# Kernel optimization log

Hardware: AMD Instinct MI355X
Metric: run time of the kernel (lower is better)

The kernel has to match this reference:

```python
import jax, jax.numpy as jnp
import numpy as np

B, S, D_IN, D_HID, D_OUT, H = 2, 2048, 1024, 1024, 1024, 16
HD = D_HID // H  # head_dim = 64


def setup_inputs() -> dict:
    key = jax.random.key(0)
    ks = jax.random.split(key, 9)
    s_in = 1.0 / np.sqrt(D_IN)
    s_out = 1.0 / np.sqrt(D_OUT)
    return {
        "x": jax.random.normal(ks[0], (B, S, D_IN), dtype=jnp.float32),
        "Wq": jax.random.uniform(ks[1], (D_IN, D_HID), jnp.float32, -s_in, s_in),
        "bq": jax.random.uniform(ks[2], (D_HID,), jnp.float32, -s_in, s_in),
        "Wk": jax.random.uniform(ks[3], (D_IN, D_HID), jnp.float32, -s_in, s_in),
        "bk": jax.random.uniform(ks[4], (D_HID,), jnp.float32, -s_in, s_in),
        "Wv": jax.random.uniform(ks[5], (D_IN, D_OUT), jnp.float32, -s_in, s_in),
        "bv": jax.random.uniform(ks[6], (D_OUT,), jnp.float32, -s_in, s_in),
        "Wo": jax.random.uniform(ks[7], (D_OUT, D_OUT), jnp.float32, -s_out, s_out),
        "bo": jax.random.uniform(ks[8], (D_OUT,), jnp.float32, -s_out, s_out),
    }


def reference(x, Wq, bq, Wk, bk, Wv, bv, Wo, bo):
    b, s, _ = x.shape
    q = (x @ Wq + bq).reshape(b, s, H, HD)  # [B,S,H,HD]
    k = (x @ Wk + bk).reshape(b, s, H, HD)
    v = (x @ Wv + bv).reshape(b, s, H, HD)
    scores = jnp.einsum("bqhd,bkhd->bhqk", q, k) / jnp.sqrt(jnp.float32(HD))
    attn = jax.nn.softmax(scores, axis=-1)  # [B,H,S,S]
    ctx = jnp.einsum("bhqk,bkhd->bqhd", attn, v).reshape(b, s, D_HID)
    return ctx @ Wo + bo
```

## Files before the change

### kernel.cpp

```cpp
#include <hip/hip_runtime.h>
#include <stdint.h>

typedef __attribute__((ext_vector_type(8))) short short8v;
typedef __attribute__((ext_vector_type(4))) short short4v;
typedef __attribute__((ext_vector_type(4))) float float4v;
typedef __attribute__((ext_vector_type(4))) unsigned short ushort4v;
typedef __attribute__((ext_vector_type(4))) float floatvec4;
typedef __attribute__((ext_vector_type(2))) unsigned int uint2v;

#define DEVI __device__ __forceinline__

DEVI unsigned short f2bf(float f) {
    unsigned int u = __builtin_bit_cast(unsigned int, f);
    u += 0x7FFFu + ((u >> 16) & 1u);
    return (unsigned short)(u >> 16);
}

DEVI unsigned int pk2bf(float a, float b) {
#if defined(__has_builtin) && __has_builtin(__builtin_amdgcn_cvt_pk_bf16_f32)
    auto r = __builtin_amdgcn_cvt_pk_bf16_f32(a, b);
    unsigned int u;
    __builtin_memcpy(&u, &r, 4);
    return u;
#else
    return (unsigned int)f2bf(a) | ((unsigned int)f2bf(b) << 16);
#endif
}

DEVI float ex2(float x) {
#if defined(__has_builtin) && __has_builtin(__builtin_amdgcn_exp2f)
    return __builtin_amdgcn_exp2f(x);
#else
    return __builtin_exp2f(x);
#endif
}

typedef __attribute__((address_space(1))) void GV;
typedef __attribute__((address_space(3))) void LV;
DEVI void gl2lds16(const void* g, void* l) {
    __builtin_amdgcn_global_load_lds((GV*)g, (LV*)l, 16, 0, 0);
}

__global__ void conv_x_kernel(const float* __restrict__ x, unsigned short* __restrict__ xb) {
    const int i = (blockIdx.x * 256 + threadIdx.x) * 4;
    const floatvec4 v = *(const floatvec4*)&x[i];
    ushort4v o;
#pragma unroll
    for (int r = 0; r < 4; r++) o[r] = f2bf(v[r]);
    *(ushort4v*)&xb[i] = o;
}

__global__ void transpose_w4(const float* __restrict__ W0, const float* __restrict__ W1,
                             const float* __restrict__ W2, const float* __restrict__ W3,
                             unsigned short* __restrict__ D0, unsigned short* __restrict__ D1,
                             unsigned short* __restrict__ D2, unsigned short* __restrict__ D3) {
    __shared__ float t[32][33];
    const int tx = threadIdx.x, ty = threadIdx.y;
    const int bx = blockIdx.x, by = blockIdx.y, z = blockIdx.z;
    const float* W = (z == 0) ? W0 : (z == 1) ? W1 : (z == 2) ? W2 : W3;
    unsigned short* D = (z == 0) ? D0 : (z == 1) ? D1 : (z == 2) ? D2 : D3;
#pragma unroll
    for (int i = 0; i < 4; i++)
        t[ty + i * 8][tx] = W[(size_t)(by * 32 + ty + i * 8) * 1024 + bx * 32 + tx];
    __syncthreads();
#pragma unroll
    for (int i = 0; i < 4; i++)
        D[(size_t)(bx * 32 + ty + i * 8) * 1024 + by * 32 + tx] = f2bf(t[tx][ty + i * 8]);
}

__global__ __launch_bounds__(256, 2) void qkv_gemm(
    const unsigned short* __restrict__ X, const unsigned short* __restrict__ Wt,
    const float* __restrict__ bq, const float* __restrict__ bk, const float* __restrict__ bv,
    unsigned short* __restrict__ qb, unsigned short* __restrict__ kb,
    unsigned short* __restrict__ vtb)
{
    __shared__ __align__(16) unsigned short As[128 * 32];
    __shared__ __align__(16) unsigned short Bs[128 * 32];
    const int tid = threadIdx.x, lane = tid & 63, wv = tid >> 6;
    const int quad = lane >> 4, l16 = lane & 15;
    const int w = blockIdx.x >> 3;
    const int n0 = (blockIdx.x & 7) * 128;
    const int row0 = blockIdx.y * 128;
    const unsigned short* Wsel = Wt + (size_t)w * (1024 * 1024);

    const int srow = lane >> 2;
    const int sg = (lane & 3) ^ ((lane >> 2) & 3) ^ ((lane >> 4) & 3);
    const int scol = sg * 8;
    const int fsw = (l16 & 3) ^ ((l16 >> 2) & 3);
    const int wm = (wv >> 1) * 64, wn = (wv & 1) * 64;

    float4v acc[4][4];
#pragma unroll
    for (int i = 0; i < 4; i++)
#pragma unroll
        for (int j = 0; j < 4; j++) acc[i][j] = (float4v){0.f, 0.f, 0.f, 0.f};

    for (int k0 = 0; k0 < 1024; k0 += 32) {
        __syncthreads();
#pragma unroll
        for (int i = 0; i < 2; i++) {
            const int c = wv * 2 + i;
            gl2lds16(X + (size_t)(row0 + c * 16 + srow) * 1024 + k0 + scol, As + c * 512);
            gl2lds16(Wsel + (size_t)(n0 + c * 16 + srow) * 1024 + k0 + scol, Bs + c * 512);
        }
        __syncthreads();
        short8v a[4], b[4];
#pragma unroll
        for (int mt = 0; mt < 4; mt++)
            a[mt] = *(const short8v*)&As[(wm + mt * 16 + l16) * 32 + ((quad ^ fsw) * 8)];
#pragma unroll
        for (int nt = 0; nt < 4; nt++)
            b[nt] = *(const short8v*)&Bs[(wn + nt * 16 + l16) * 32 + ((quad ^ fsw) * 8)];
#pragma unroll
        for (int mt = 0; mt < 4; mt++)
#pragma unroll
            for (int nt = 0; nt < 4; nt++)
                acc[mt][nt] = __builtin_amdgcn_mfma_f32_16x16x32_bf16(a[mt], b[nt], acc[mt][nt], 0, 0, 0);
    }

    const float* bias = (w == 0) ? bq : (w == 1) ? bk : bv;
    const float scl = (w == 0) ? 0.18033688011112042f : 1.0f;
#pragma unroll
    for (int nt = 0; nt < 4; nt++) {
        const int col = n0 + wn + nt * 16 + l16;
        const float bb = bias[col];
        const int h = col >> 6, hd = col & 63;
#pragma unroll
        for (int mt = 0; mt < 4; mt++) {
            const int tok0 = row0 + wm + mt * 16 + quad * 4;
            const int b_ = tok0 >> 11, s0 = tok0 & 2047;
            if (w == 2) {
                ushort4v pk;
#pragma unroll
                for (int r = 0; r < 4; r++) pk[r] = f2bf(acc[mt][nt][r] + bb);
                *(ushort4v*)&vtb[(((size_t)b_ * 16 + h) * 64 + hd) * 2048 + s0] = pk;
            } else {
                unsigned short* dst = (w == 0) ? qb : kb;
#pragma unroll
                for (int r = 0; r < 4; r++)
                    dst[(((size_t)b_ * 16 + h) * 2048 + (s0 + r)) * 64 + hd] =
                        f2bf((acc[mt][nt][r] + bb) * scl);
            }
        }
    }
}

__global__ __launch_bounds__(256, 4) void attn_kernel(
    const unsigned short* __restrict__ qb, const unsigned short* __restrict__ kb,
    const unsigned short* __restrict__ vtb, unsigned short* __restrict__ ctxb)
{
    __shared__ __align__(16) unsigned short Kt[128 * 64];
    __shared__ __align__(16) unsigned short Vt[64 * 128];
    __shared__ __align__(16) unsigned short Pbs[4][32 * 32];
    const int tid = threadIdx.x, lane = tid & 63, wv = tid >> 6;
    const int quad = lane >> 4, l16 = lane & 15;
    const int bh = blockIdx.x, qt = blockIdx.y;
    const size_t boff = (size_t)bh * (2048 * 64);
    const unsigned short* qp = qb + boff;
    const unsigned short* kp = kb + boff;
    const unsigned short* vp = vtb + boff;
    const int q0 = qt * 128 + wv * 32;

    short8v qf[2][2];
#pragma unroll
    for (int nt = 0; nt < 2; nt++)
#pragma unroll
        for (int kc = 0; kc < 2; kc++)
            qf[nt][kc] = *(const short8v*)&qp[(size_t)(q0 + nt * 16 + l16) * 64 + kc * 32 + quad * 8];

    float4v accO[2][4];
#pragma unroll
    for (int nt = 0; nt < 2; nt++)
#pragma unroll
        for (int ht = 0; ht < 4; ht++) accO[nt][ht] = (float4v){0.f, 0.f, 0.f, 0.f};
    float lsum[2] = {0.f, 0.f};

    const int krow = lane >> 3;
    const int kg = (lane & 7) ^ (lane >> 3);
    const int vrow = lane >> 4;
    const int rsw = l16 & 7;

    const int ktb0 = l16 * 64 + ((quad ^ rsw) * 8);
    const int ktb1 = l16 * 64 + (((4 + quad) ^ rsw) * 8);
    const int vrb = l16 * 128 + ((quad ^ (l16 & 3)) * 8);
    const int l12e = (l16 & 12) * 8;
    const int pwb = l16 * 32 + ((quad ^ ((l16 >> 1) & 3)) * 4);
    const int hsw = (l16 >> 3) & 1;
    const int s1 = (l16 >> 1) & 1;
    const int prbase = l16 * 32 + ((quad ^ ((l16 >> 2) & 3)) * 8);
    const int pr0 = prbase + s1 * 4;
    const int pr1 = prbase + (1 - s1) * 4;

    for (int kt0 = 0; kt0 < 2048; kt0 += 128) {
        __syncthreads();
#pragma unroll
        for (int i = 0; i < 4; i++) {
            const int c = wv * 4 + i;
            gl2lds16(kp + (size_t)(kt0 + c * 8 + krow) * 64 + kg * 8, Kt + c * 512);
            const int vr = c * 4 + vrow;
            const int vg = (lane & 15) ^ (vr & 15);
            gl2lds16(vp + (size_t)vr * 2048 + kt0 + vg * 8, Vt + c * 512);
        }
        __syncthreads();

#pragma unroll
        for (int kc = 0; kc < 4; kc++) {
#pragma unroll
            for (int h = 0; h < 2; h++) {
                const int mt = kc * 2 + h;
                const short8v a0 = *(const short8v*)&Kt[ktb0 + mt * 1024];
                const short8v a1 = *(const short8v*)&Kt[ktb1 + mt * 1024];
                const int hoff = (h ^ hsw) * 16;
#pragma unroll
                for (int nt = 0; nt < 2; nt++) {
                    float4v z = (float4v){0.f, 0.f, 0.f, 0.f};
                    z = __builtin_amdgcn_mfma_f32_16x16x32_bf16(a0, qf[nt][0], z, 0, 0, 0);
                    z = __builtin_amdgcn_mfma_f32_16x16x32_bf16(a1, qf[nt][1], z, 0, 0, 0);
                    const float p0 = ex2(z[0]), p1 = ex2(z[1]);
                    const float p2 = ex2(z[2]), p3 = ex2(z[3]);
                    lsum[nt] += (p0 + p1) + (p2 + p3);
                    *(uint2v*)&Pbs[wv][pwb + hoff + nt * 512] =
                        (uint2v){pk2bf(p0, p1), pk2bf(p2, p3)};
                }
            }
            short8v bvv[4];
            const int roff = (kc * 32) ^ l12e;
#pragma unroll
            for (int ht = 0; ht < 4; ht++)
                bvv[ht] = *(const short8v*)&Vt[vrb + roff + ht * 2048];
            asm volatile("s_waitcnt lgkmcnt(0)" ::: "memory");
#pragma unroll
            for (int nt = 0; nt < 2; nt++) {
                const short4v d0 = *(const short4v*)&Pbs[wv][pr0 + nt * 512];
                const short4v d1 = *(const short4v*)&Pbs[wv][pr1 + nt * 512];
                const short8v ap = __builtin_shufflevector(d0, d1, 0, 1, 2, 3, 4, 5, 6, 7);
#pragma unroll
                for (int ht = 0; ht < 4; ht++)
                    accO[nt][ht] = __builtin_amdgcn_mfma_f32_16x16x32_bf16(ap, bvv[ht], accO[nt][ht], 0, 0, 0);
            }
        }
    }

#pragma unroll
    for (int nt = 0; nt < 2; nt++) {
        lsum[nt] += __shfl_xor(lsum[nt], 16);
        lsum[nt] += __shfl_xor(lsum[nt], 32);
    }

    const int b_ = bh >> 4, h = bh & 15;
#pragma unroll
    for (int nt = 0; nt < 2; nt++)
#pragma unroll
        for (int r = 0; r < 4; r++) {
            const int s = q0 + nt * 16 + quad * 4 + r;
            const float inv = 1.0f / __shfl(lsum[nt], quad * 4 + r);
#pragma unroll
            for (int ht = 0; ht < 4; ht++) {
                const int hd = ht * 16 + l16;
                ctxb[((size_t)(b_ * 2048 + s)) * 1024 + h * 64 + hd] = f2bf(accO[nt][ht][r] * inv);
            }
        }
}

__global__ __launch_bounds__(256, 2) void out_gemm(
    const unsigned short* __restrict__ ctx, const unsigned short* __restrict__ Wot,
    const float* __restrict__ bo, float* __restrict__ out)
{
    __shared__ __align__(16) unsigned short As[128 * 32];
    __shared__ __align__(16) unsigned short Bs[128 * 32];
    const int tid = threadIdx.x, lane = tid & 63, wv = tid >> 6;
    const int quad = lane >> 4, l16 = lane & 15;
    const int n0 = blockIdx.x * 128;
    const int row0 = blockIdx.y * 128;

    const int srow = lane >> 2;
    const int sg = (lane & 3) ^ ((lane >> 2) & 3) ^ ((lane >> 4) & 3);
    const int scol = sg * 8;
    const int fsw = (l16 & 3) ^ ((l16 >> 2) & 3);
    const int wm = (wv >> 1) * 64, wn = (wv & 1) * 64;

    float4v acc[4][4];
#pragma unroll
    for (int i = 0; i < 4; i++)
#pragma unroll
        for (int j = 0; j < 4; j++) acc[i][j] = (float4v){0.f, 0.f, 0.f, 0.f};

    for (int k0 = 0; k0 < 1024; k0 += 32) {
        __syncthreads();
#pragma unroll
        for (int i = 0; i < 2; i++) {
            const int c = wv * 2 + i;
            gl2lds16(ctx + (size_t)(row0 + c * 16 + srow) * 1024 + k0 + scol, As + c * 512);
            gl2lds16(Wot + (size_t)(n0 + c * 16 + srow) * 1024 + k0 + scol, Bs + c * 512);
        }
        __syncthreads();
        short8v a[4], b[4];
#pragma unroll
        for (int mt = 0; mt < 4; mt++)
            a[mt] = *(const short8v*)&As[(wm + mt * 16 + l16) * 32 + ((quad ^ fsw) * 8)];
#pragma unroll
        for (int nt = 0; nt < 4; nt++)
            b[nt] = *(const short8v*)&Bs[(wn + nt * 16 + l16) * 32 + ((quad ^ fsw) * 8)];
#pragma unroll
        for (int mt = 0; mt < 4; mt++)
#pragma unroll
            for (int nt = 0; nt < 4; nt++)
                acc[mt][nt] = __builtin_amdgcn_mfma_f32_16x16x32_bf16(a[mt], b[nt], acc[mt][nt], 0, 0, 0);
    }

#pragma unroll
    for (int nt = 0; nt < 4; nt++) {
        const int col = n0 + wn + nt * 16 + l16;
        const float bb = bo[col];
#pragma unroll
        for (int mt = 0; mt < 4; mt++) {
            const int tok0 = row0 + wm + mt * 16 + quad * 4;
#pragma unroll
            for (int r = 0; r < 4; r++)
                out[(size_t)(tok0 + r) * 1024 + col] = acc[mt][nt][r] + bb;
        }
    }
}

extern "C" void kernel_launch(void* const* d_in, const int* in_sizes, int n_in,
                              void* d_out, int out_size, void* d_ws, size_t ws_size,
                              hipStream_t stream) {
    const float* x  = (const float*)d_in[0];
    const float* Wq = (const float*)d_in[1];
    const float* bq = (const float*)d_in[2];
    const float* Wk = (const float*)d_in[3];
    const float* bk = (const float*)d_in[4];
    const float* Wv = (const float*)d_in[5];
    const float* bv = (const float*)d_in[6];
    const float* Wo = (const float*)d_in[7];
    const float* bo = (const float*)d_in[8];
    float* out = (float*)d_out;

    char* ws = (char*)d_ws;
    unsigned short* xb   = (unsigned short*)(ws);
    unsigned short* qbuf = (unsigned short*)(ws + (8u << 20));
    unsigned short* kbuf = (unsigned short*)(ws + (16u << 20));
    unsigned short* vtb  = (unsigned short*)(ws + (24u << 20));
    unsigned short* wt   = (unsigned short*)(ws + (32u << 20));
    unsigned short* wot  = (unsigned short*)(ws + (38u << 20));

    conv_x_kernel<<<4096, 256, 0, stream>>>(x, xb);
    transpose_w4<<<dim3(32, 32, 4), dim3(32, 8), 0, stream>>>(
        Wq, Wk, Wv, Wo, wt, wt + (1u << 20), wt + (2u << 20), wot);

    qkv_gemm<<<dim3(24, 32), 256, 0, stream>>>(xb, wt, bq, bk, bv, qbuf, kbuf, vtb);
    attn_kernel<<<dim3(32, 16), 256, 0, stream>>>(qbuf, kbuf, vtb, xb );
    out_gemm<<<dim3(8, 32), 256, 0, stream>>>(xb, wot, bo, out);
}
```

Before: 220.6 us.

## Merge prep kernels, deepen QKV K-tile, restructure attention P buffer, shrink out-GEMM tiles

Measured after the change: 196.8 us. -10.8%, faster.

```diff
diff --git a/kernel.cpp b/kernel.cpp
--- a/kernel.cpp
+++ b/kernel.cpp
@@ -41,22 +41,26 @@
     __builtin_amdgcn_global_load_lds((GV*)g, (LV*)l, 16, 0, 0);
 }
 
-__global__ void conv_x_kernel(const float* __restrict__ x, unsigned short* __restrict__ xb) {
-    const int i = (blockIdx.x * 256 + threadIdx.x) * 4;
-    const floatvec4 v = *(const floatvec4*)&x[i];
-    ushort4v o;
-#pragma unroll
-    for (int r = 0; r < 4; r++) o[r] = f2bf(v[r]);
-    *(ushort4v*)&xb[i] = o;
-}
-
-__global__ void transpose_w4(const float* __restrict__ W0, const float* __restrict__ W1,
-                             const float* __restrict__ W2, const float* __restrict__ W3,
-                             unsigned short* __restrict__ D0, unsigned short* __restrict__ D1,
-                             unsigned short* __restrict__ D2, unsigned short* __restrict__ D3) {
+__global__ void prep_kernel(const float* __restrict__ x, unsigned short* __restrict__ xb,
+                            const float* __restrict__ W0, const float* __restrict__ W1,
+                            const float* __restrict__ W2, const float* __restrict__ W3,
+                            unsigned short* __restrict__ D0, unsigned short* __restrict__ D1,
+                            unsigned short* __restrict__ D2, unsigned short* __restrict__ D3) {
+    const int bid = blockIdx.x, tid = threadIdx.x;
+    if (bid < 4096) {
+        const int i = (bid * 256 + tid) * 4;
+        const floatvec4 v = *(const floatvec4*)&x[i];
+        ushort4v o;
+#pragma unroll
+        for (int r = 0; r < 4; r++) o[r] = f2bf(v[r]);
+        *(ushort4v*)&xb[i] = o;
+        return;
+    }
     __shared__ float t[32][33];
-    const int tx = threadIdx.x, ty = threadIdx.y;
-    const int bx = blockIdx.x, by = blockIdx.y, z = blockIdx.z;
+    const int tcode = bid - 4096;
+    const int z = tcode >> 10, rem = tcode & 1023;
+    const int by = rem >> 5, bx = rem & 31;
+    const int tx = tid & 31, ty = tid >> 5;
     const float* W = (z == 0) ? W0 : (z == 1) ? W1 : (z == 2) ? W2 : W3;
     unsigned short* D = (z == 0) ? D0 : (z == 1) ? D1 : (z == 2) ? D2 : D3;
 #pragma unroll
@@ -68,14 +72,14 @@
         D[(size_t)(bx * 32 + ty + i * 8) * 1024 + by * 32 + tx] = f2bf(t[tx][ty + i * 8]);
 }
 
-__global__ __launch_bounds__(256, 2) void qkv_gemm(
+__global__ __launch_bounds__(256, 3) void qkv_gemm(
     const unsigned short* __restrict__ X, const unsigned short* __restrict__ Wt,
     const float* __restrict__ bq, const float* __restrict__ bk, const float* __restrict__ bv,
     unsigned short* __restrict__ qb, unsigned short* __restrict__ kb,
     unsigned short* __restrict__ vtb)
 {
-    __shared__ __align__(16) unsigned short As[128 * 32];
-    __shared__ __align__(16) unsigned short Bs[128 * 32];
+    __shared__ __align__(16) unsigned short As[128 * 64];
+    __shared__ __align__(16) unsigned short Bs[128 * 64];
     const int tid = threadIdx.x, lane = tid & 63, wv = tid >> 6;
     const int quad = lane >> 4, l16 = lane & 15;
     const int w = blockIdx.x >> 3;
@@ -83,10 +87,9 @@
     const int row0 = blockIdx.y * 128;
     const unsigned short* Wsel = Wt + (size_t)w * (1024 * 1024);
 
-    const int srow = lane >> 2;
-    const int sg = (lane & 3) ^ ((lane >> 2) & 3) ^ ((lane >> 4) & 3);
-    const int scol = sg * 8;
-    const int fsw = (l16 & 3) ^ ((l16 >> 2) & 3);
+    const int srow = lane >> 3;
+    const int qsc = ((lane & 7) ^ (lane >> 3 & 7)) * 8;
+    const int fsw = l16 & 7;
     const int wm = (wv >> 1) * 64, wn = (wv & 1) * 64;
 
     float4v acc[4][4];
@@ -95,27 +98,31 @@
 #pragma unroll
         for (int j = 0; j < 4; j++) acc[i][j] = (float4v){0.f, 0.f, 0.f, 0.f};
 
-    for (int k0 = 0; k0 < 1024; k0 += 32) {
-        __syncthreads();
-#pragma unroll
-        for (int i = 0; i < 2; i++) {
-            const int c = wv * 2 + i;
-            gl2lds16(X + (size_t)(row0 + c * 16 + srow) * 1024 + k0 + scol, As + c * 512);
-            gl2lds16(Wsel + (size_t)(n0 + c * 16 + srow) * 1024 + k0 + scol, Bs + c * 512);
-        }
-        __syncthreads();
-        short8v a[4], b[4];
-#pragma unroll
-        for (int mt = 0; mt < 4; mt++)
-            a[mt] = *(const short8v*)&As[(wm + mt * 16 + l16) * 32 + ((quad ^ fsw) * 8)];
-#pragma unroll
-        for (int nt = 0; nt < 4; nt++)
-            b[nt] = *(const short8v*)&Bs[(wn + nt * 16 + l16) * 32 + ((quad ^ fsw) * 8)];
-#pragma unroll
-        for (int mt = 0; mt < 4; mt++)
+    for (int k0 = 0; k0 < 1024; k0 += 64) {
+        __syncthreads();
+#pragma unroll
+        for (int i = 0; i < 4; i++) {
+            const int c = wv * 4 + i;
+            gl2lds16(X + (size_t)(row0 + c * 8 + srow) * 1024 + k0 + qsc, As + c * 512);
+            gl2lds16(Wsel + (size_t)(n0 + c * 8 + srow) * 1024 + k0 + qsc, Bs + c * 512);
+        }
+        __syncthreads();
+#pragma unroll
+        for (int kc = 0; kc < 2; kc++) {
+            const int sl = (((kc * 4 + quad) ^ fsw) * 8);
+            short8v a[4], b[4];
+#pragma unroll
+            for (int mt = 0; mt < 4; mt++)
+                a[mt] = *(const short8v*)&As[(wm + mt * 16 + l16) * 64 + sl];
 #pragma unroll
             for (int nt = 0; nt < 4; nt++)
-                acc[mt][nt] = __builtin_amdgcn_mfma_f32_16x16x32_bf16(a[mt], b[nt], acc[mt][nt], 0, 0, 0);
+                b[nt] = *(const short8v*)&Bs[(wn + nt * 16 + l16) * 64 + sl];
+#pragma unroll
+            for (int mt = 0; mt < 4; mt++)
+#pragma unroll
+                for (int nt = 0; nt < 4; nt++)
+                    acc[mt][nt] = __builtin_amdgcn_mfma_f32_16x16x32_bf16(a[mt], b[nt], acc[mt][nt], 0, 0, 0);
+        }
     }
 
     const float* bias = (w == 0) ? bq : (w == 1) ? bk : bv;
@@ -145,13 +152,13 @@
     }
 }
 
-__global__ __launch_bounds__(256, 4) void attn_kernel(
+__global__ __launch_bounds__(256, 2) void attn_kernel(
     const unsigned short* __restrict__ qb, const unsigned short* __restrict__ kb,
     const unsigned short* __restrict__ vtb, unsigned short* __restrict__ ctxb)
 {
     __shared__ __align__(16) unsigned short Kt[128 * 64];
     __shared__ __align__(16) unsigned short Vt[64 * 128];
-    __shared__ __align__(16) unsigned short Pbs[4][32 * 32];
+    __shared__ __align__(16) unsigned short Pb[4][32 * 128];
     const int tid = threadIdx.x, lane = tid & 63, wv = tid >> 6;
     const int quad = lane >> 4, l16 = lane & 15;
     const int bh = blockIdx.x, qt = blockIdx.y;
@@ -184,12 +191,7 @@
     const int ktb1 = l16 * 64 + (((4 + quad) ^ rsw) * 8);
     const int vrb = l16 * 128 + ((quad ^ (l16 & 3)) * 8);
     const int l12e = (l16 & 12) * 8;
-    const int pwb = l16 * 32 + ((quad ^ ((l16 >> 1) & 3)) * 4);
-    const int hsw = (l16 >> 3) & 1;
-    const int s1 = (l16 >> 1) & 1;
-    const int prbase = l16 * 32 + ((quad ^ ((l16 >> 2) & 3)) * 8);
-    const int pr0 = prbase + s1 * 4;
-    const int pr1 = prbase + (1 - s1) * 4;
+    const int prow = l16 * 128;
 
     for (int kt0 = 0; kt0 < 2048; kt0 += 128) {
         __syncthreads();
@@ -204,35 +206,36 @@
         __syncthreads();
 
 #pragma unroll
+        for (int mt = 0; mt < 8; mt++) {
+            const short8v a0 = *(const short8v*)&Kt[ktb0 + mt * 1024];
+            const short8v a1 = *(const short8v*)&Kt[ktb1 + mt * 1024];
+            const int pwo = prow + (((mt * 4 + quad) ^ l16) * 4);
+#pragma unroll
+            for (int nt = 0; nt < 2; nt++) {
+                float4v z = (float4v){0.f, 0.f, 0.f, 0.f};
+                z = __builtin_amdgcn_mfma_f32_16x16x32_bf16(a0, qf[nt][0], z, 0, 0, 0);
+                z = __builtin_amdgcn_mfma_f32_16x16x32_bf16(a1, qf[nt][1], z, 0, 0, 0);
+                const float p0 = ex2(z[0]), p1 = ex2(z[1]);
+                const float p2 = ex2(z[2]), p3 = ex2(z[3]);
+                lsum[nt] += (p0 + p1) + (p2 + p3);
+                *(uint2v*)&Pb[wv][pwo + nt * 2048] = (uint2v){pk2bf(p0, p1), pk2bf(p2, p3)};
+            }
+        }
+        asm volatile("s_waitcnt lgkmcnt(0)" ::: "memory");
+
+#pragma unroll
         for (int kc = 0; kc < 4; kc++) {
-#pragma unroll
-            for (int h = 0; h < 2; h++) {
-                const int mt = kc * 2 + h;
-                const short8v a0 = *(const short8v*)&Kt[ktb0 + mt * 1024];
-                const short8v a1 = *(const short8v*)&Kt[ktb1 + mt * 1024];
-                const int hoff = (h ^ hsw) * 16;
-#pragma unroll
-                for (int nt = 0; nt < 2; nt++) {
-                    float4v z = (float4v){0.f, 0.f, 0.f, 0.f};
-                    z = __builtin_amdgcn_mfma_f32_16x16x32_bf16(a0, qf[nt][0], z, 0, 0, 0);
-                    z = __builtin_amdgcn_mfma_f32_16x16x32_bf16(a1, qf[nt][1], z, 0, 0, 0);
-                    const float p0 = ex2(z[0]), p1 = ex2(z[1]);
-                    const float p2 = ex2(z[2]), p3 = ex2(z[3]);
-                    lsum[nt] += (p0 + p1) + (p2 + p3);
-                    *(uint2v*)&Pbs[wv][pwb + hoff + nt * 512] =
-                        (uint2v){pk2bf(p0, p1), pk2bf(p2, p3)};
-                }
-            }
+            const int roff = (kc * 32) ^ l12e;
             short8v bvv[4];
-            const int roff = (kc * 32) ^ l12e;
 #pragma unroll
             for (int ht = 0; ht < 4; ht++)
                 bvv[ht] = *(const short8v*)&Vt[vrb + roff + ht * 2048];
-            asm volatile("s_waitcnt lgkmcnt(0)" ::: "memory");
+            const int c0 = prow + (((kc * 8 + quad * 2) ^ l16) * 4);
+            const int c1 = prow + (((kc * 8 + quad * 2 + 1) ^ l16) * 4);
 #pragma unroll
             for (int nt = 0; nt < 2; nt++) {
-                const short4v d0 = *(const short4v*)&Pbs[wv][pr0 + nt * 512];
-                const short4v d1 = *(const short4v*)&Pbs[wv][pr1 + nt * 512];
+                const short4v d0 = *(const short4v*)&Pb[wv][c0 + nt * 2048];
+                const short4v d1 = *(const short4v*)&Pb[wv][c1 + nt * 2048];
                 const short8v ap = __builtin_shufflevector(d0, d1, 0, 1, 2, 3, 4, 5, 6, 7);
 #pragma unroll
                 for (int ht = 0; ht < 4; ht++)
@@ -262,58 +265,61 @@
         }
 }
 
-__global__ __launch_bounds__(256, 2) void out_gemm(
+__global__ __launch_bounds__(256, 4) void out_gemm(
     const unsigned short* __restrict__ ctx, const unsigned short* __restrict__ Wot,
     const float* __restrict__ bo, float* __restrict__ out)
 {
-    __shared__ __align__(16) unsigned short As[128 * 32];
-    __shared__ __align__(16) unsigned short Bs[128 * 32];
+    __shared__ __align__(16) unsigned short As[64 * 32];
+    __shared__ __align__(16) unsigned short Bs[64 * 32];
     const int tid = threadIdx.x, lane = tid & 63, wv = tid >> 6;
     const int quad = lane >> 4, l16 = lane & 15;
-    const int n0 = blockIdx.x * 128;
-    const int row0 = blockIdx.y * 128;
+    const int n0 = blockIdx.x * 64;
+    const int row0 = blockIdx.y * 64;
 
     const int srow = lane >> 2;
     const int sg = (lane & 3) ^ ((lane >> 2) & 3) ^ ((lane >> 4) & 3);
     const int scol = sg * 8;
     const int fsw = (l16 & 3) ^ ((l16 >> 2) & 3);
-    const int wm = (wv >> 1) * 64, wn = (wv & 1) * 64;
-
-    float4v acc[4][4];
-#pragma unroll
-    for (int i = 0; i < 4; i++)
-#pragma unroll
-        for (int j = 0; j < 4; j++) acc[i][j] = (float4v){0.f, 0.f, 0.f, 0.f};
+    const int wm = (wv & 1) * 32, wn = (wv >> 1) * 32;
+
+    float4v acc[2][2];
+#pragma unroll
+    for (int i = 0; i < 2; i++)
+#pragma unroll
+        for (int j = 0; j < 2; j++) acc[i][j] = (float4v){0.f, 0.f, 0.f, 0.f};
 
     for (int k0 = 0; k0 < 1024; k0 += 32) {
         __syncthreads();
 #pragma unroll
         for (int i = 0; i < 2; i++) {
-            const int c = wv * 2 + i;
-            gl2lds16(ctx + (size_t)(row0 + c * 16 + srow) * 1024 + k0 + scol, As + c * 512);
-            gl2lds16(Wot + (size_t)(n0 + c * 16 + srow) * 1024 + k0 + scol, Bs + c * 512);
-        }
-        __syncthreads();
-        short8v a[4], b[4];
-#pragma unroll
-        for (int mt = 0; mt < 4; mt++)
+            const int idx = wv * 2 + i;
+            if (idx < 4)
+                gl2lds16(ctx + (size_t)(row0 + idx * 16 + srow) * 1024 + k0 + scol, As + idx * 512);
+            else
+                gl2lds16(Wot + (size_t)(n0 + (idx - 4) * 16 + srow) * 1024 + k0 + scol,
+                         Bs + (idx - 4) * 512);
+        }
+        __syncthreads();
+        short8v a[2], b[2];
+#pragma unroll
+        for (int mt = 0; mt < 2; mt++)
             a[mt] = *(const short8v*)&As[(wm + mt * 16 + l16) * 32 + ((quad ^ fsw) * 8)];
 #pragma unroll
-        for (int nt = 0; nt < 4; nt++)
+        for (int nt = 0; nt < 2; nt++)
             b[nt] = *(const short8v*)&Bs[(wn + nt * 16 + l16) * 32 + ((quad ^ fsw) * 8)];
 #pragma unroll
-        for (int mt = 0; mt < 4; mt++)
-#pragma unroll
-            for (int nt = 0; nt < 4; nt++)
+        for (int mt = 0; mt < 2; mt++)
+#pragma unroll
+            for (int nt = 0; nt < 2; nt++)
                 acc[mt][nt] = __builtin_amdgcn_mfma_f32_16x16x32_bf16(a[mt], b[nt], acc[mt][nt], 0, 0, 0);
     }
 
 #pragma unroll
-    for (int nt = 0; nt < 4; nt++) {
+    for (int nt = 0; nt < 2; nt++) {
         const int col = n0 + wn + nt * 16 + l16;
         const float bb = bo[col];
 #pragma unroll
-        for (int mt = 0; mt < 4; mt++) {
+        for (int mt = 0; mt < 2; mt++) {
             const int tok0 = row0 + wm + mt * 16 + quad * 4;
 #pragma unroll
             for (int r = 0; r < 4; r++)
@@ -344,11 +350,9 @@
     unsigned short* wt   = (unsigned short*)(ws + (32u << 20));
     unsigned short* wot  = (unsigned short*)(ws + (38u << 20));
 
-    conv_x_kernel<<<4096, 256, 0, stream>>>(x, xb);
-    transpose_w4<<<dim3(32, 32, 4), dim3(32, 8), 0, stream>>>(
-        Wq, Wk, Wv, Wo, wt, wt + (1u << 20), wt + (2u << 20), wot);
-
+    prep_kernel<<<8192, 256, 0, stream>>>(x, xb, Wq, Wk, Wv, Wo,
+                                          wt, wt + (1u << 20), wt + (2u << 20), wot);
     qkv_gemm<<<dim3(24, 32), 256, 0, stream>>>(xb, wt, bq, bk, bv, qbuf, kbuf, vtb);
     attn_kernel<<<dim3(32, 16), 256, 0, stream>>>(qbuf, kbuf, vtb, xb );
-    out_gemm<<<dim3(8, 32), 256, 0, stream>>>(xb, wot, bo, out);
-}
+    out_gemm<<<dim3(16, 64), 256, 0, stream>>>(xb, wot, bo, out);
+}
```
